# Performance work log

Hardware: AMD Instinct MI355X
Metric: run time of the kernel (lower is better)

## Reference

```python
import jax, jax.numpy as jnp
import numpy as np

T, B, S, K, C = 2, 64, 30, 12, 20
N_ITEMS, D_ITEM, D_RNN = 20000, 128, 256
D_IN = D_ITEM + D_RNN  # cross_mode concatenates h_meta to basket embedding


def gru_cell(x, h, Wih, Whh, bih, bhh):
    # PyTorch GRUCell gate order: r, z, n
    gi = x @ Wih.T + bih
    gh = h @ Whh.T + bhh
    ir, iz, in_ = jnp.split(gi, 3, -1)
    hr, hz, hn = jnp.split(gh, 3, -1)
    r = jax.nn.sigmoid(ir + hr)
    z = jax.nn.sigmoid(iz + hz)
    n = jnp.tanh(in_ + r * hn)
    return (1.0 - z) * n + z * h


def setup_inputs() -> dict:
    key = jax.random.key(0)
    ks = jax.random.split(key, 16)
    def u(k, sh, fan):
        b = 1.0 / np.sqrt(fan)
        return jax.random.uniform(k, sh, jnp.float32, -b, b)
    return {
        "user_vectors": jax.random.randint(ks[0], (B,), 0, 1000),
        "item_vectors": jax.random.randint(ks[1], (T, B, S, K), 0, N_ITEMS),
        "copy_vectors": jax.random.randint(ks[2], (T, B, S, C), 0, N_ITEMS),
        "emb": jax.random.normal(ks[3], (N_ITEMS, D_ITEM), jnp.float32) * 0.05,
        "Wih": u(ks[4], (T, 3 * D_RNN, D_IN), D_RNN),
        "Whh": u(ks[5], (T, 3 * D_RNN, D_RNN), D_RNN),
        "bih": u(ks[6], (T, 3 * D_RNN), D_RNN),
        "bhh": u(ks[7], (T, 3 * D_RNN), D_RNN),
        "mWih": u(ks[8], (3 * D_RNN, T * D_RNN), D_RNN),
        "mWhh": u(ks[9], (3 * D_RNN, D_RNN), D_RNN),
        "mbih": u(ks[10], (3 * D_RNN,), D_RNN),
        "mbhh": u(ks[11], (3 * D_RNN,), D_RNN),
        "Wnew": u(ks[12], (N_ITEMS, D_RNN), D_RNN),
        "bnew": u(ks[13], (N_ITEMS,), D_RNN),
        "Wcopy": u(ks[14], (T, N_ITEMS, D_RNN), D_RNN),
        "bcopy": u(ks[15], (T, N_ITEMS), D_RNN),
    }


def _forward(item_vectors, copy_vectors, emb, Wih, Whh, bih, bhh,
             mWih, mWhh, mbih, mbhh, Wnew, bnew, Wcopy, bcopy):
    emb = emb.at[0].set(0.0)  # padding_idx=0
    e_items = emb[item_vectors]                               # [T,B,S,K,Di]
    valid = (item_vectors > 0).astype(e_items.dtype)          # [T,B,S,K]
    n_basket = valid.sum(-1)                                  # [T,B,S]
    cell_mask = (n_basket > 0).astype(e_items.dtype)          # [T,B,S]
    den = n_basket + (n_basket == 0).astype(e_items.dtype)
    e_baskets = e_items.sum(-2) / den[..., None]              # ave pool [T,B,S,Di]

    xs = jnp.moveaxis(e_baskets, 2, 0)  # [S,T,B,Di]
    ms = jnp.moveaxis(cell_mask, 2, 0)  # [S,T,B]

    h0 = jnp.zeros((T, B, D_RNN), e_items.dtype)
    hm0 = jnp.zeros((B, D_RNN), e_items.dtype)
    task_gru = jax.vmap(gru_cell)  # vmap over the task axis (distinct weights)

    def step(carry, inp):
        h_tasks, h_meta = carry
        x_t, m_t = inp
        # cross_mode: concat current meta hidden onto each task's input
        cell_in = jnp.concatenate(
            [x_t, jnp.broadcast_to(h_meta, (T, B, D_RNN))], -1)  # [T,B,D_IN]
        nh = task_gru(cell_in, h_tasks, Wih, Whh, bih, bhh)
        m = m_t[..., None]
        h_tasks = nh * m + h_tasks * (1.0 - m)  # freeze hidden on empty baskets
        meta_in = jnp.transpose(h_tasks, (1, 0, 2)).reshape(B, T * D_RNN)
        h_meta = gru_cell(meta_in, h_meta, mWih, mWhh, mbih, mbhh)
        return (h_tasks, h_meta), (h_tasks, h_meta)

    _, (h_seq, hm_seq) = jax.lax.scan(step, (h0, hm0), (xs, ms))
    e_rnn_tasks = jnp.transpose(h_seq, (1, 2, 0, 3))  # [T,B,S,H]
    e_rnn_meta = jnp.transpose(hm_seq, (1, 0, 2))     # [B,S,H]

    score_new = jnp.einsum('bsh,nh->bsn', e_rnn_meta, Wnew) + bnew  # [B,S,N]
    ti = jnp.arange(T)[:, None, None, None]
    bi = jnp.arange(B)[None, :, None, None]
    si = jnp.arange(S)[None, None, :, None]
    copy_mask = jnp.zeros((T, B, S, N_ITEMS), score_new.dtype).at[
        ti, bi, si, copy_vectors].set(1.0)  # scatter_(-1, copy_vectors, 1)
    score_copy = (jnp.einsum('tbsh,tnh->tbsn', e_rnn_tasks, Wcopy)
                  + bcopy[:, None, None, :]) * copy_mask  # [T,B,S,N]
    # stack new-item scores with per-task masked copy scores
    return jnp.concatenate([score_new[None], score_copy], 0)  # [T+1,B,S,N]


def reference(user_vectors, item_vectors, copy_vectors, emb, Wih, Whh, bih, bhh,
              mWih, mWhh, mbih, mbhh, Wnew, bnew, Wcopy, bcopy):
    return _forward(item_vectors, copy_vectors, emb, Wih, Whh, bih, bhh,
                    mWih, mWhh, mbih, mbhh, Wnew, bnew, Wcopy, bcopy)
```

## Files before the change

kernel.cpp:

```cpp
#include <hip/hip_runtime.h>

typedef unsigned short u16;
typedef unsigned int u32;
typedef unsigned long long u64;
typedef __attribute__((ext_vector_type(8))) short short8;
typedef __attribute__((ext_vector_type(4))) float f32x4;

#define NB_ 64
#define HELPERS_ 1152

static __device__ __forceinline__ f32x4 mfma16(short8 a, short8 b, f32x4 c) {
  return __builtin_amdgcn_mfma_f32_16x16x32_bf16(a, b, c, 0, 0, 0);
}

static __device__ __forceinline__ void split_bf16(float x, u16& hi, u16& lo) {
  unsigned u = __float_as_uint(x);
  unsigned r = (u + 0x7fffu + ((u >> 16) & 1u)) >> 16;
  hi = (u16)r;
  float fh = __uint_as_float(r << 16);
  float xl = x - fh;
  unsigned ul = __float_as_uint(xl);
  unsigned rl2 = (ul + 0x7fffu + ((ul >> 16) & 1u)) >> 16;
  lo = (u16)rl2;
}

static __device__ __forceinline__ void astore(u32* p, u32 v) {
  __hip_atomic_store(p, v, __ATOMIC_RELAXED, __HIP_MEMORY_SCOPE_AGENT);
}
static __device__ __forceinline__ void unpack8(const uint4& a, const uint4& b,
                                               short8& h, short8& l) {
  u32 wb[8] = {a.x, a.y, a.z, a.w, b.x, b.y, b.z, b.w};
  #pragma unroll
  for (int j = 0; j < 8; ++j) {
    h[j] = (short)(wb[j] & 0xffffu);
    l[j] = (short)(wb[j] >> 16);
  }
}
static __device__ __forceinline__ float unpack_hl(u32 pk) {
  return __uint_as_float((pk & 0xffffu) << 16) + __uint_as_float(pk & 0xffff0000u);
}
static __device__ __forceinline__ void vload8(const u32* p, short8& h, short8& l) {
  uint4 a = *(const uint4*)p;
  uint4 b = *(const uint4*)(p + 4);
  unpack8(a, b, h, l);
}

__global__ __launch_bounds__(128) void k_pool(const int* __restrict__ iv,
                                              const float* __restrict__ emb,
                                              u16* __restrict__ ebh, u16* __restrict__ ebl,
                                              float* __restrict__ cm) {
  int u = blockIdx.x;
  int s = u >> 7;
  int t = (u >> 6) & 1;
  int b = u & 63;
  int d = threadIdx.x;
  const int ibase = ((t * 64 + b) * 30 + s) * 12;
  float sum = 0.f;
  int cnt = 0;
  for (int k = 0; k < 12; ++k) {
    int idx = iv[ibase + k];
    if (idx > 0) { cnt++; sum += emb[(size_t)idx * 128 + d]; }
  }
  float den = (cnt > 0) ? (float)cnt : 1.f;
  float v = sum / den;
  u16 hi, lo; split_bf16(v, hi, lo);
  ebh[(size_t)u * 128 + d] = hi;
  ebl[(size_t)u * 128 + d] = lo;
  if (d == 0) cm[u] = (cnt > 0) ? 1.f : 0.f;
}

__global__ __launch_bounds__(256) void k_swz(const float* __restrict__ Wih,
                                             const float* __restrict__ Whh,
                                             const float* __restrict__ mWih,
                                             const float* __restrict__ mWhh,
                                             const float* __restrict__ Wnew,
                                             u16* __restrict__ w1h, u16* __restrict__ w1l,
                                             u16* __restrict__ w2h, u16* __restrict__ w2l,
                                             u16* __restrict__ wnh, u16* __restrict__ wnl) {
  int gu = blockIdx.x * 4 + (threadIdx.x >> 6);
  int lane = threadIdx.x & 63;
  int ko = (lane >> 4) * 8;
  int cl = lane & 15;
  float src[8];
  if (gu < 2560) {
    int blk = gu / 40, r = gu % 40, ksIdx = r >> 1, nt = r & 1;
    int t = blk >> 5, hd0 = (blk & 31) * 8;
    int c = nt * 16 + cl;
    if (c < 24) {
      int gc = (c < 8) ? (hd0 + c) : (c < 16) ? (256 + hd0 + (c - 8)) : (512 + hd0 + (c - 16));
      const float* wrow; int kk;
      if (ksIdx < 8)       { wrow = Wih + (size_t)(t * 768 + gc) * 384 + 128; kk = ksIdx * 32 + ko; }
      else if (ksIdx < 16) { wrow = Whh + (size_t)(t * 768 + gc) * 256;       kk = (ksIdx - 8) * 32 + ko; }
      else                 { wrow = Wih + (size_t)(t * 768 + gc) * 384;       kk = (ksIdx - 16) * 32 + ko; }
      #pragma unroll
      for (int j = 0; j < 8; ++j) src[j] = wrow[kk + j];
    } else {
      #pragma unroll
      for (int j = 0; j < 8; ++j) src[j] = 0.f;
    }
    int off = gu * 512 + lane * 8;
    #pragma unroll
    for (int j = 0; j < 8; ++j) { u16 h, l; split_bf16(src[j], h, l); w1h[off + j] = h; w1l[off + j] = l; }
  } else if (gu < 4096) {
    int g2 = gu - 2560;
    int blk = g2 / 24, ksIdx = g2 % 24;
    int t1 = blk >> 5;
    int hd0 = blk * 4;
    int c = cl;
    if (c < 12) {
      int gc = (c < 4) ? (hd0 + c) : (c < 8) ? (256 + hd0 + (c - 4)) : (512 + hd0 + (c - 8));
      if (ksIdx < 16) {
        int chunk = (ksIdx < 8) ? (t1 * 8 + ksIdx) : ((1 - t1) * 8 + (ksIdx - 8));
        int kk = chunk * 32 + ko;
        #pragma unroll
        for (int j = 0; j < 8; ++j) src[j] = mWih[(size_t)gc * 512 + kk + j];
      } else {
        int kk = (ksIdx - 16) * 32 + ko;
        #pragma unroll
        for (int j = 0; j < 8; ++j) src[j] = mWhh[(size_t)gc * 256 + kk + j];
      }
    } else {
      #pragma unroll
      for (int j = 0; j < 8; ++j) src[j] = 0.f;
    }
    int off = g2 * 512 + lane * 8;
    #pragma unroll
    for (int j = 0; j < 8; ++j) { u16 h, l; split_bf16(src[j], h, l); w2h[off + j] = h; w2l[off + j] = l; }
  } else if (gu < 14144) {
    int g3 = gu - 4096;
    int gnt = g3 >> 3, ks = g3 & 7;
    int col = gnt * 16 + cl;
    if (col < 20000) {
      int kk = ks * 32 + ko;
      #pragma unroll
      for (int j = 0; j < 8; ++j) src[j] = Wnew[(size_t)col * 256 + kk + j];
    } else {
      #pragma unroll
      for (int j = 0; j < 8; ++j) src[j] = 0.f;
    }
    int off = g3 * 512 + lane * 8;
    #pragma unroll
    for (int j = 0; j < 8; ++j) { u16 h, l; split_bf16(src[j], h, l); wnh[off + j] = h; wnl[off + j] = l; }
  }
}

__global__ __launch_bounds__(256) void k_gix(const u16* __restrict__ ebh, const u16* __restrict__ ebl,
                                             const u16* __restrict__ w1h, const u16* __restrict__ w1l,
                                             const float* __restrict__ bih, const float* __restrict__ bhh,
                                             float* __restrict__ gix) {
  int blk = blockIdx.x;
  int t1 = blk >> 5, hd1 = (blk & 31) * 8;
  int tid = threadIdx.x, lane = tid & 63, w = tid >> 6;
  int arow = w * 16 + (lane & 15);
  int ko = (lane >> 4) * 8;
  __shared__ u16 lwh[4096], lwl[4096];
  {
    const uint4* sh = (const uint4*)(w1h + ((size_t)blk * 40 + 32) * 512);
    const uint4* sl = (const uint4*)(w1l + ((size_t)blk * 40 + 32) * 512);
    uint4* dh = (uint4*)lwh; uint4* dl = (uint4*)lwl;
    for (int i = tid; i < 512; i += 256) { dh[i] = sh[i]; dl[i] = sl[i]; }
  }
  int c = lane & 15;
  float brz, bn = 0.f;
  {
    int gc = (c < 8) ? (hd1 + c) : (256 + hd1 + (c - 8));
    brz = bih[t1 * 768 + gc] + bhh[t1 * 768 + gc];
    if (c < 8) bn = bih[t1 * 768 + 512 + hd1 + c];
  }
  __syncthreads();
  for (int s = 0; s < 30; ++s) {
    f32x4 a3[2];
    a3[0] = (f32x4){0.f, 0.f, 0.f, 0.f};
    a3[1] = (f32x4){0.f, 0.f, 0.f, 0.f};
    const u16* Xh = ebh + (size_t)((s * 2 + t1) * 64 + arow) * 128;
    const u16* Xl = ebl + (size_t)((s * 2 + t1) * 64 + arow) * 128;
    #pragma unroll
    for (int k = 0; k < 4; ++k) {
      short8 xh = *(const short8*)(Xh + k * 32 + ko);
      short8 xl = *(const short8*)(Xl + k * 32 + ko);
      #pragma unroll
      for (int nt = 0; nt < 2; ++nt) {
        short8 bh = *(const short8*)(lwh + (k * 2 + nt) * 512 + lane * 8);
        short8 bl = *(const short8*)(lwl + (k * 2 + nt) * 512 + lane * 8);
        a3[nt] = mfma16(xh, bh, a3[nt]);
        a3[nt] = mfma16(xl, bh, a3[nt]);
        a3[nt] = mfma16(xh, bl, a3[nt]);
      }
    }
    float* grow = gix + (size_t)(blk * 30 + s) * 64 * 32;
    #pragma unroll
    for (int i = 0; i < 4; ++i) {
      int r = w * 16 + (lane >> 4) * 4 + i;
      grow[r * 32 + c] = a3[0][i] + brz;
      if (c < 8) grow[r * 32 + 16 + c] = a3[1][i] + bn;
    }
  }
}

static __device__ __forceinline__ void bar_arrive(u32* slots, int blk, int epoch) {
  __syncthreads();
  if (threadIdx.x == 0) astore(slots + blk, (u32)epoch);
}
static __device__ __forceinline__ void bar_wait(u32* slots, int epoch) {
  int lane = threadIdx.x & 63;
  u32 v;
  for (;;) {
    asm volatile("global_load_dword %0, %1, off sc0 sc1\n\ts_waitcnt vmcnt(0)"
                 : "=v"(v) : "v"(slots + lane) : "memory");
    if ((int)v >= epoch) break;
  }
}

#define RNN_LDS 130560

__global__ __launch_bounds__(256, 1) void k_rnn(
    const u16* __restrict__ w1h, const u16* __restrict__ w1l,
    const u16* __restrict__ w2h, const u16* __restrict__ w2l,
    const float* __restrict__ gix,
    const float* __restrict__ bhh,
    const float* __restrict__ mbih, const float* __restrict__ mbhh,
    const float* __restrict__ cm,
    u32* __restrict__ hpk,
    u32* __restrict__ apk,
    u32* slots,
    float* __restrict__ zout) {
  if (blockIdx.x >= NB_) {
    const size_t totalf4 = 19200000;
    size_t idx = (size_t)(blockIdx.x - NB_) * 256 + threadIdx.x;
    size_t stride = (size_t)HELPERS_ * 256;
    f32x4 z4 = {0.f, 0.f, 0.f, 0.f};
    f32x4* zp = (f32x4*)zout;
    for (size_t i = idx; i < totalf4; i += stride)
      __builtin_nontemporal_store(z4, zp + i);
    return;
  }

  extern __shared__ char smem[];
  u16* lw1h = (u16*)smem;
  u16* lw1l = (u16*)(smem + 32768);
  u16* lw2h = (u16*)(smem + 65536);
  u16* lw2l = (u16*)(smem + 90112);
  float* ls_rz = (float*)(smem + 114688);
  float* ls_gi = (float*)(smem + 118784);
  float* ls_gh = (float*)(smem + 120832);
  float* ls_cm = (float*)(smem + 122880);

  const int blk = blockIdx.x;
  const int tid = threadIdx.x;
  const int lane = tid & 63;
  const int w = tid >> 6;
  const int t1 = blk >> 5;
  const int hd1 = (blk & 31) * 8;
  const int hd2 = blk * 4;
  const int arow = w * 16 + (lane & 15);
  const int ko = (lane >> 4) * 8;
  int epoch = 0;

  {
    const uint4* s1h = (const uint4*)(w1h + (size_t)blk * 40 * 512);
    const uint4* s1l = (const uint4*)(w1l + (size_t)blk * 40 * 512);
    uint4* d1h = (uint4*)lw1h; uint4* d1l = (uint4*)lw1l;
    for (int i = tid; i < 2048; i += 256) { d1h[i] = s1h[i]; d1l[i] = s1l[i]; }
    const uint4* s2h = (const uint4*)(w2h + (size_t)blk * 24 * 512);
    const uint4* s2l = (const uint4*)(w2l + (size_t)blk * 24 * 512);
    uint4* d2h = (uint4*)lw2h; uint4* d2l = (uint4*)lw2l;
    for (int i = tid; i < 1536; i += 256) { d2h[i] = s2h[i]; d2l[i] = s2l[i]; }
    for (int i = tid; i < 1920; i += 256) ls_cm[i] = cm[((i >> 6) * 2 + t1) * 64 + (i & 63)];
  }
  const int cc = lane & 15;
  float bhhn = (cc < 8) ? bhh[t1 * 768 + 512 + hd1 + cc] : 0.f;
  float mrz_b = 0.f, mgi_b = 0.f, mgh_b = 0.f;
  if (cc < 8) {
    int gc = (cc < 4) ? (hd2 + cc) : (256 + hd2 + (cc - 4));
    mrz_b = mbih[gc] + mbhh[gc];
  } else if (cc < 12) {
    int gn = 512 + hd2 + (cc - 8);
    mgi_b = mbih[gn];
    mgh_b = mbhh[gn];
  }

  float gq[8];
  {
    const float* grow = gix + (size_t)(blk * 30 + 0) * 2048;
    #pragma unroll
    for (int i = 0; i < 4; ++i) {
      int r = w * 16 + (lane >> 4) * 4 + i;
      gq[i]     = grow[r * 32 + cc];
      gq[4 + i] = grow[r * 32 + 16 + (cc & 7)];
    }
  }
  __syncthreads();

  short8 ah1[8], al1[8];
  short8 xh2[8], xl2[8];
  f32x4 a2s[2];
  a2s[0] = (f32x4){0.f, 0.f, 0.f, 0.f};
  a2s[1] = (f32x4){0.f, 0.f, 0.f, 0.f};
  float hold0 = 0.f, hold1 = 0.f;
  float hm_reg = 0.f;

  for (int s = 0; s < 30; ++s) {
    f32x4 a1[2];
    a1[0] = (f32x4){0.f, 0.f, 0.f, 0.f};
    a1[1] = (f32x4){0.f, 0.f, 0.f, 0.f};
    if (s > 0) {
      bar_wait(slots, epoch);
      const u32* Ap = apk + (size_t)(arow * 30 + (s - 1)) * 256 + ko;
      uint4 ra[16];
      #pragma unroll
      for (int k = 0; k < 8; ++k) {
        ra[2 * k]     = *(const uint4*)(Ap + k * 32);
        ra[2 * k + 1] = *(const uint4*)(Ap + k * 32 + 4);
      }
      #pragma unroll
      for (int k = 0; k < 8; ++k) {
        unpack8(ra[2 * k], ra[2 * k + 1], ah1[k], al1[k]);
        #pragma unroll
        for (int nt = 0; nt < 2; ++nt) {
          short8 bh = *(const short8*)(lw1h + (k * 2 + nt) * 512 + lane * 8);
          short8 bl = *(const short8*)(lw1l + (k * 2 + nt) * 512 + lane * 8);
          a1[nt] = mfma16(ah1[k], bh, a1[nt]);
          a1[nt] = mfma16(al1[k], bh, a1[nt]);
          a1[nt] = mfma16(ah1[k], bl, a1[nt]);
        }
      }
    }
    #pragma unroll
    for (int i = 0; i < 4; ++i) {
      int rl = (lane >> 4) * 4 + i;
      ls_rz[(w * 16 + rl) * 16 + cc] = a1[0][i] + a2s[0][i] + gq[i];
      if (cc < 8) {
        ls_gi[(w * 16 + rl) * 8 + cc] = a1[1][i] + gq[4 + i];
        ls_gh[(w * 16 + rl) * 8 + cc] = a2s[1][i] + bhhn;
      }
    }
    asm volatile("s_waitcnt lgkmcnt(0)" ::: "memory");
    {
      int item = lane;
      int rl = item >> 3, c = item & 7;
      float rv = ls_rz[(w * 16 + rl) * 16 + c], zv = ls_rz[(w * 16 + rl) * 16 + 8 + c];
      float gi = ls_gi[(w * 16 + rl) * 8 + c], gh = ls_gh[(w * 16 + rl) * 8 + c];
      float r = 1.f / (1.f + expf(-rv));
      float z = 1.f / (1.f + expf(-zv));
      float n = tanhf(gi + r * gh);
      int b = w * 16 + rl;
      float m = ls_cm[s * 64 + b];
      float hnew = (1.f - z) * n + z * hold0;
      float hout = (m > 0.5f) ? hnew : hold0;
      hold0 = hout;
      int oo = (((s + 1) * 2 + t1) * 64 + b) * 256 + hd1 + c;
      u16 xh, xl; split_bf16(hout, xh, xl);
      astore(hpk + oo, (u32)xh | ((u32)xl << 16));
    }
    {
      int item = 64 + lane;
      int rl = item >> 3, c = item & 7;
      float rv = ls_rz[(w * 16 + rl) * 16 + c], zv = ls_rz[(w * 16 + rl) * 16 + 8 + c];
      float gi = ls_gi[(w * 16 + rl) * 8 + c], gh = ls_gh[(w * 16 + rl) * 8 + c];
      float r = 1.f / (1.f + expf(-rv));
      float z = 1.f / (1.f + expf(-zv));
      float n = tanhf(gi + r * gh);
      int b = w * 16 + rl;
      float m = ls_cm[s * 64 + b];
      float hnew = (1.f - z) * n + z * hold1;
      float hout = (m > 0.5f) ? hnew : hold1;
      hold1 = hout;
      int oo = (((s + 1) * 2 + t1) * 64 + b) * 256 + hd1 + c;
      u16 xh, xl; split_bf16(hout, xh, xl);
      astore(hpk + oo, (u32)xh | ((u32)xl << 16));
    }
    ++epoch;
    bar_arrive(slots, blk, epoch);

    f32x4 m1 = (f32x4){0.f, 0.f, 0.f, 0.f};
    f32x4 m2 = (f32x4){0.f, 0.f, 0.f, 0.f};
    if (s > 0) {
      #pragma unroll
      for (int k = 0; k < 8; ++k) {
        short8 bh = *(const short8*)(lw2h + (16 + k) * 512 + lane * 8);
        short8 bl = *(const short8*)(lw2l + (16 + k) * 512 + lane * 8);
        m2 = mfma16(ah1[k], bh, m2);
        m2 = mfma16(al1[k], bh, m2);
        m2 = mfma16(ah1[k], bl, m2);
      }
    }
    if (s < 29) {
      const float* grow = gix + (size_t)(blk * 30 + s + 1) * 2048;
      #pragma unroll
      for (int i = 0; i < 4; ++i) {
        int r = w * 16 + (lane >> 4) * 4 + i;
        gq[i]     = grow[r * 32 + cc];
        gq[4 + i] = grow[r * 32 + 16 + (cc & 7)];
      }
    }
    bar_wait(slots, epoch);

    {
      const u32* Hp = hpk + (size_t)(((s + 1) * 2 + t1) * 64 + arow) * 256 + ko;
      const u32* Hq = hpk + (size_t)(((s + 1) * 2 + (1 - t1)) * 64 + arow) * 256 + ko;
      uint4 rx[16], ry[16];
      #pragma unroll
      for (int k = 0; k < 8; ++k) {
        rx[2 * k]     = *(const uint4*)(Hp + k * 32);
        rx[2 * k + 1] = *(const uint4*)(Hp + k * 32 + 4);
        ry[2 * k]     = *(const uint4*)(Hq + k * 32);
        ry[2 * k + 1] = *(const uint4*)(Hq + k * 32 + 4);
      }
      #pragma unroll
      for (int k = 0; k < 8; ++k) {
        unpack8(rx[2 * k], rx[2 * k + 1], xh2[k], xl2[k]);
        short8 bh = *(const short8*)(lw2h + k * 512 + lane * 8);
        short8 bl = *(const short8*)(lw2l + k * 512 + lane * 8);
        m1 = mfma16(xh2[k], bh, m1);
        m1 = mfma16(xl2[k], bh, m1);
        m1 = mfma16(xh2[k], bl, m1);
      }
      #pragma unroll
      for (int k = 0; k < 8; ++k) {
        short8 yh, yl;
        unpack8(ry[2 * k], ry[2 * k + 1], yh, yl);
        short8 bh = *(const short8*)(lw2h + (8 + k) * 512 + lane * 8);
        short8 bl = *(const short8*)(lw2l + (8 + k) * 512 + lane * 8);
        m1 = mfma16(yh, bh, m1);
        m1 = mfma16(yl, bh, m1);
        m1 = mfma16(yh, bl, m1);
      }
    }
    #pragma unroll
    for (int i = 0; i < 4; ++i) {
      int rl = (lane >> 4) * 4 + i;
      if (cc < 8) {
        ls_rz[(w * 16 + rl) * 16 + cc] = m1[i] + m2[i] + mrz_b;
      } else if (cc < 12) {
        ls_gi[(w * 16 + rl) * 8 + (cc - 8)] = m1[i] + mgi_b;
        ls_gh[(w * 16 + rl) * 8 + (cc - 8)] = m2[i] + mgh_b;
      }
    }
    asm volatile("s_waitcnt lgkmcnt(0)" ::: "memory");
    {
      int rl = lane >> 2, c = lane & 3;
      float rv = ls_rz[(w * 16 + rl) * 16 + c], zv = ls_rz[(w * 16 + rl) * 16 + 4 + c];
      float gi = ls_gi[(w * 16 + rl) * 8 + c], gh = ls_gh[(w * 16 + rl) * 8 + c];
      float r = 1.f / (1.f + expf(-rv));
      float z = 1.f / (1.f + expf(-zv));
      float n = tanhf(gi + r * gh);
      int b = w * 16 + rl;
      int g2 = hd2 + c;
      float hmnew = (1.f - z) * n + z * hm_reg;
      hm_reg = hmnew;
      int ar = b * 30 + s;
      u16 xh, xl; split_bf16(hmnew, xh, xl);
      astore(apk + ar * 256 + g2, (u32)xh | ((u32)xl << 16));
    }
    ++epoch;
    bar_arrive(slots, blk, epoch);

    a2s[0] = (f32x4){0.f, 0.f, 0.f, 0.f};
    a2s[1] = (f32x4){0.f, 0.f, 0.f, 0.f};
    if (s < 29) {
      #pragma unroll
      for (int k = 0; k < 8; ++k) {
        #pragma unroll
        for (int nt = 0; nt < 2; ++nt) {
          short8 bh = *(const short8*)(lw1h + ((8 + k) * 2 + nt) * 512 + lane * 8);
          short8 bl = *(const short8*)(lw1l + ((8 + k) * 2 + nt) * 512 + lane * 8);
          a2s[nt] = mfma16(xh2[k], bh, a2s[nt]);
          a2s[nt] = mfma16(xl2[k], bh, a2s[nt]);
          a2s[nt] = mfma16(xh2[k], bl, a2s[nt]);
        }
      }
    }
  }
}

__global__ __launch_bounds__(256) void k_gnew(const u32* __restrict__ apk,
                                              const u16* __restrict__ wnh, const u16* __restrict__ wnl,
                                              const float* __restrict__ bnew,
                                              float* __restrict__ out) {
  int bid = blockIdx.x;
  int mb = bid / 157, nb = bid % 157;
  int tid = threadIdx.x, lane = tid & 63, w = tid >> 6;
  int ko = (lane >> 4) * 8;
  f32x4 acc[2][8];
  #pragma unroll
  for (int mi = 0; mi < 2; ++mi)
    #pragma unroll
    for (int nt = 0; nt < 8; ++nt) acc[mi][nt] = (f32x4){0.f, 0.f, 0.f, 0.f};
  #pragma unroll
  for (int ks = 0; ks < 8; ++ks) {
    short8 ah[2], al[2];
    #pragma unroll
    for (int mi = 0; mi < 2; ++mi) {
      int r = mb * 128 + (w * 2 + mi) * 16 + (lane & 15);
      vload8(apk + (size_t)r * 256 + ks * 32 + ko, ah[mi], al[mi]);
    }
    #pragma unroll
    for (int nt = 0; nt < 8; ++nt) {
      int un = (nb * 8 + nt) * 8 + ks;
      short8 bh = *(const short8*)(wnh + (size_t)un * 512 + lane * 8);
      short8 bl = *(const short8*)(wnl + (size_t)un * 512 + lane * 8);
      #pragma unroll
      for (int mi = 0; mi < 2; ++mi) {
        acc[mi][nt] = mfma16(ah[mi], bh, acc[mi][nt]);
        acc[mi][nt] = mfma16(al[mi], bh, acc[mi][nt]);
        acc[mi][nt] = mfma16(ah[mi], bl, acc[mi][nt]);
      }
    }
  }
  #pragma unroll
  for (int mi = 0; mi < 2; ++mi)
    #pragma unroll
    for (int nt = 0; nt < 8; ++nt) {
      int col = nb * 128 + nt * 16 + (lane & 15);
      if (col < 20000) {
        float bn = bnew[col];
        #pragma unroll
        for (int i = 0; i < 4; ++i) {
          int r = mb * 128 + (w * 2 + mi) * 16 + (lane >> 4) * 4 + i;
          out[(size_t)r * 20000 + col] = acc[mi][nt][i] + bn;
        }
      }
    }
}

__global__ __launch_bounds__(256) void k_copy(const u32* __restrict__ hpk,
                                              const int* __restrict__ cv,
                                              const float* __restrict__ wc,
                                              const float* __restrict__ bc,
                                              float* __restrict__ out) {
  int u = blockIdx.x;
  int t = u / 1920;
  int rem = u % 1920;
  int b = rem / 30, s = rem % 30;
  int tid = threadIdx.x, lane = tid & 63, w = tid >> 6;
  float* orow = out + (size_t)(1 + t) * 38400000 + (size_t)(b * 30 + s) * 20000;
  const u32* hp = hpk + (size_t)(((s + 1) * 2 + t) * 64 + b) * 256;
  uint4 hq = *(const uint4*)(hp + lane * 4);
  float4 h4;
  h4.x = unpack_hl(hq.x); h4.y = unpack_hl(hq.y);
  h4.z = unpack_hl(hq.z); h4.w = unpack_hl(hq.w);
  int base = u * 20;
  for (int c = w; c < 20; c += 4) {
    int idx = cv[base + c];
    const float* wr = wc + ((size_t)t * 20000 + idx) * 256;
    float4 w4 = *(const float4*)(wr + lane * 4);
    float d = h4.x * w4.x + h4.y * w4.y + h4.z * w4.z + h4.w * w4.w;
    #pragma unroll
    for (int m = 32; m >= 1; m >>= 1) d += __shfl_xor(d, m, 64);
    if (lane == 0) orow[idx] = d + bc[t * 20000 + idx];
  }
}

extern "C" void kernel_launch(void* const* d_in, const int* in_sizes, int n_in,
                              void* d_out, int out_size, void* d_ws, size_t ws_size,
                              hipStream_t stream) {
  const int* iv = (const int*)d_in[1];
  const int* cv = (const int*)d_in[2];
  const float* emb = (const float*)d_in[3];
  const float* Wih = (const float*)d_in[4];
  const float* Whh = (const float*)d_in[5];
  const float* bih = (const float*)d_in[6];
  const float* bhh = (const float*)d_in[7];
  const float* mWih = (const float*)d_in[8];
  const float* mWhh = (const float*)d_in[9];
  const float* mbih = (const float*)d_in[10];
  const float* mbhh = (const float*)d_in[11];
  const float* Wnew = (const float*)d_in[12];
  const float* bnew = (const float*)d_in[13];
  const float* Wcopy = (const float*)d_in[14];
  const float* bcopy = (const float*)d_in[15];
  float* out = (float*)d_out;
  char* ws = (char*)d_ws;

  size_t o = 0;
  auto take = [&](size_t sz) { size_t r = o; o += sz; return r; };
  size_t BAR = take(256);
  size_t CM  = take(15360);
  size_t EBH = take(983040);
  size_t EBL = take(983040);
  size_t HPK = take(4063232);
  size_t APK = take(1966080);
  size_t GIX = take(15728640);
  size_t W1H = take(2621440);
  size_t W1L = take(2621440);
  size_t W2H = take(1572864);
  size_t W2L = take(1572864);
  size_t WNH = take(10289152);
  size_t WNL = take(10289152);
  if (ws_size < o) return;

  hipFuncSetAttribute(reinterpret_cast<const void*>(k_rnn),
                      hipFuncAttributeMaxDynamicSharedMemorySize, RNN_LDS);

  hipMemsetAsync(ws + BAR, 0, 256, stream);

  k_pool<<<3840, 128, 0, stream>>>(iv, emb, (u16*)(ws + EBH), (u16*)(ws + EBL), (float*)(ws + CM));
  k_swz<<<3536, 256, 0, stream>>>(Wih, Whh, mWih, mWhh, Wnew,
                                  (u16*)(ws + W1H), (u16*)(ws + W1L),
                                  (u16*)(ws + W2H), (u16*)(ws + W2L),
                                  (u16*)(ws + WNH), (u16*)(ws + WNL));
  k_gix<<<64, 256, 0, stream>>>((const u16*)(ws + EBH), (const u16*)(ws + EBL),
                                (const u16*)(ws + W1H), (const u16*)(ws + W1L),
                                bih, bhh, (float*)(ws + GIX));
  k_rnn<<<NB_ + HELPERS_, 256, RNN_LDS, stream>>>(
      (const u16*)(ws + W1H), (const u16*)(ws + W1L),
      (const u16*)(ws + W2H), (const u16*)(ws + W2L),
      (const float*)(ws + GIX), bhh, mbih, mbhh,
      (const float*)(ws + CM),
      (u32*)(ws + HPK), (u32*)(ws + APK),
      (u32*)(ws + BAR),
      out + 38400000);
  k_gnew<<<2355, 256, 0, stream>>>((const u32*)(ws + APK),
                                   (const u16*)(ws + WNH), (const u16*)(ws + WNL),
                                   bnew, out);
  k_copy<<<3840, 256, 0, stream>>>((const u32*)(ws + HPK), cv, Wcopy, bcopy, out);
}
```

Before: 574.1 us.

## Fuse output GEMM and copy scoring into RNN kernel as epoch-gated helper blocks

The separate new-item GEMM and copy-score kernels are folded into the persistent RNN launch as helper blocks. Each helper zeroes its output rows, then spin-waits (with sleeps) on the RNN barrier epoch for the timestep it needs, so output work overlaps the sequential recurrence instead of running after it. The meta hidden-state buffer is changed to timestep-major so each 128-row GEMM tile depends only on two timesteps. The risk is that waiting helpers each hold a CU (the kernel requests about 130 KB of LDS, so one block per CU) and rely on in-order dispatch to avoid starving the RNN blocks.

Result: faster. 488.9 us (-14.8%).

```diff
diff --git a/kernel.cpp b/kernel.cpp
--- a/kernel.cpp
+++ b/kernel.cpp
@@ -7,7 +7,7 @@
 typedef __attribute__((ext_vector_type(4))) float f32x4;
 
 #define NB_ 64
-#define HELPERS_ 1152
+#define NHELP_ 6195
 
 static __device__ __forceinline__ f32x4 mfma16(short8 a, short8 b, f32x4 c) {
   return __builtin_amdgcn_mfma_f32_16x16x32_bf16(a, b, c, 0, 0, 0);
@@ -210,10 +210,23 @@
     if ((int)v >= epoch) break;
   }
 }
+static __device__ __forceinline__ void helper_wait(u32* slots, int target) {
+  if (threadIdx.x < 64) {
+    u32 v;
+    for (;;) {
+      asm volatile("global_load_dword %0, %1, off sc0 sc1\n\ts_waitcnt vmcnt(0)"
+                   : "=v"(v) : "v"(slots + threadIdx.x) : "memory");
+      if (__all((int)v >= target)) break;
+      __builtin_amdgcn_s_sleep(15);
+      __builtin_amdgcn_s_sleep(15);
+    }
+  }
+  __syncthreads();
+}
 
 #define RNN_LDS 130560
 
-__global__ __launch_bounds__(256, 1) void k_rnn(
+__global__ __launch_bounds__(256, 1) void k_mega(
     const u16* __restrict__ w1h, const u16* __restrict__ w1l,
     const u16* __restrict__ w2h, const u16* __restrict__ w2l,
     const float* __restrict__ gix,
@@ -223,15 +236,88 @@
     u32* __restrict__ hpk,
     u32* __restrict__ apk,
     u32* slots,
-    float* __restrict__ zout) {
+    const u16* __restrict__ wnh, const u16* __restrict__ wnl,
+    const float* __restrict__ bnew,
+    const int* __restrict__ cv,
+    const float* __restrict__ wc,
+    const float* __restrict__ bc,
+    float* __restrict__ out) {
+
   if (blockIdx.x >= NB_) {
-    const size_t totalf4 = 19200000;
-    size_t idx = (size_t)(blockIdx.x - NB_) * 256 + threadIdx.x;
-    size_t stride = (size_t)HELPERS_ * 256;
-    f32x4 z4 = {0.f, 0.f, 0.f, 0.f};
-    f32x4* zp = (f32x4*)zout;
-    for (size_t i = idx; i < totalf4; i += stride)
-      __builtin_nontemporal_store(z4, zp + i);
+    int h = blockIdx.x - NB_;
+    int g = h / 413, r = h % 413;
+    int tid = threadIdx.x, lane = tid & 63, w = tid >> 6;
+    int ko = (lane >> 4) * 8;
+    if (r < 256) {
+      int s = 2 * g + (r >= 128);
+      int rr = r & 127;
+      int t = rr >> 6, b = rr & 63;
+      float* orow = out + (size_t)(1 + t) * 38400000 + (size_t)(b * 30 + s) * 20000;
+      f32x4 z4 = {0.f, 0.f, 0.f, 0.f};
+      f32x4* zp = (f32x4*)orow;
+      for (int i = tid; i < 5000; i += 256)
+        __builtin_nontemporal_store(z4, zp + i);
+      helper_wait(slots, 2 * s + 1);
+      const u32* hp = hpk + (size_t)(((s + 1) * 2 + t) * 64 + b) * 256;
+      uint4 hq = *(const uint4*)(hp + lane * 4);
+      float4 h4;
+      h4.x = unpack_hl(hq.x); h4.y = unpack_hl(hq.y);
+      h4.z = unpack_hl(hq.z); h4.w = unpack_hl(hq.w);
+      int base = ((t * 64 + b) * 30 + s) * 20;
+      for (int c = w; c < 20; c += 4) {
+        int idx = cv[base + c];
+        const float* wr = wc + ((size_t)t * 20000 + idx) * 256;
+        float4 w4 = *(const float4*)(wr + lane * 4);
+        float d = h4.x * w4.x + h4.y * w4.y + h4.z * w4.z + h4.w * w4.w;
+        #pragma unroll
+        for (int m = 32; m >= 1; m >>= 1) d += __shfl_xor(d, m, 64);
+        if (lane == 0) orow[idx] = d + bc[t * 20000 + idx];
+      }
+    } else {
+      int q = g, nb = r - 256;
+      helper_wait(slots, 4 * q + 4);
+      f32x4 acc[2][8];
+      #pragma unroll
+      for (int mi = 0; mi < 2; ++mi)
+        #pragma unroll
+        for (int nt = 0; nt < 8; ++nt) acc[mi][nt] = (f32x4){0.f, 0.f, 0.f, 0.f};
+      #pragma unroll
+      for (int ks = 0; ks < 8; ++ks) {
+        short8 ah[2], al[2];
+        #pragma unroll
+        for (int mi = 0; mi < 2; ++mi) {
+          int rrow = q * 128 + (w * 2 + mi) * 16 + (lane & 15);
+          vload8(apk + (size_t)rrow * 256 + ks * 32 + ko, ah[mi], al[mi]);
+        }
+        #pragma unroll
+        for (int nt = 0; nt < 8; ++nt) {
+          int un = (nb * 8 + nt) * 8 + ks;
+          short8 bh = *(const short8*)(wnh + (size_t)un * 512 + lane * 8);
+          short8 bl = *(const short8*)(wnl + (size_t)un * 512 + lane * 8);
+          #pragma unroll
+          for (int mi = 0; mi < 2; ++mi) {
+            acc[mi][nt] = mfma16(ah[mi], bh, acc[mi][nt]);
+            acc[mi][nt] = mfma16(al[mi], bh, acc[mi][nt]);
+            acc[mi][nt] = mfma16(ah[mi], bl, acc[mi][nt]);
+          }
+        }
+      }
+      #pragma unroll
+      for (int mi = 0; mi < 2; ++mi)
+        #pragma unroll
+        for (int nt = 0; nt < 8; ++nt) {
+          int col = nb * 128 + nt * 16 + (lane & 15);
+          if (col < 20000) {
+            float bn = bnew[col];
+            #pragma unroll
+            for (int i = 0; i < 4; ++i) {
+              int rrow = q * 128 + (w * 2 + mi) * 16 + (lane >> 4) * 4 + i;
+              int sA = rrow >> 6, bA = rrow & 63;
+              out[(size_t)(bA * 30 + sA) * 20000 + col] = acc[mi][nt][i] + bn;
+            }
+          }
+        }
+    }
     return;
   }
 
@@ -305,7 +391,7 @@
     a1[1] = (f32x4){0.f, 0.f, 0.f, 0.f};
     if (s > 0) {
       bar_wait(slots, epoch);
-      const u32* Ap = apk + (size_t)(arow * 30 + (s - 1)) * 256 + ko;
+      const u32* Ap = apk + (size_t)((s - 1) * 64 + arow) * 256 + ko;
       uint4 ra[16];
       #pragma unroll
       for (int k = 0; k < 8; ++k) {
@@ -448,7 +534,7 @@
       int g2 = hd2 + c;
       float hmnew = (1.f - z) * n + z * hm_reg;
       hm_reg = hmnew;
-      int ar = b * 30 + s;
+      int ar = s * 64 + b;
       u16 xh, xl; split_bf16(hmnew, xh, xl);
       astore(apk + ar * 256 + g2, (u32)xh | ((u32)xl << 16));
     }
@@ -470,84 +556,6 @@
         }
       }
     }
-  }
-}
-
-__global__ __launch_bounds__(256) void k_gnew(const u32* __restrict__ apk,
-                                              const u16* __restrict__ wnh, const u16* __restrict__ wnl,
-                                              const float* __restrict__ bnew,
-                                              float* __restrict__ out) {
-  int bid = blockIdx.x;
-  int mb = bid / 157, nb = bid % 157;
-  int tid = threadIdx.x, lane = tid & 63, w = tid >> 6;
-  int ko = (lane >> 4) * 8;
-  f32x4 acc[2][8];
-  #pragma unroll
-  for (int mi = 0; mi < 2; ++mi)
-    #pragma unroll
-    for (int nt = 0; nt < 8; ++nt) acc[mi][nt] = (f32x4){0.f, 0.f, 0.f, 0.f};
-  #pragma unroll
-  for (int ks = 0; ks < 8; ++ks) {
-    short8 ah[2], al[2];
-    #pragma unroll
-    for (int mi = 0; mi < 2; ++mi) {
-      int r = mb * 128 + (w * 2 + mi) * 16 + (lane & 15);
-      vload8(apk + (size_t)r * 256 + ks * 32 + ko, ah[mi], al[mi]);
-    }
-    #pragma unroll
-    for (int nt = 0; nt < 8; ++nt) {
-      int un = (nb * 8 + nt) * 8 + ks;
-      short8 bh = *(const short8*)(wnh + (size_t)un * 512 + lane * 8);
-      short8 bl = *(const short8*)(wnl + (size_t)un * 512 + lane * 8);
-      #pragma unroll
-      for (int mi = 0; mi < 2; ++mi) {
-        acc[mi][nt] = mfma16(ah[mi], bh, acc[mi][nt]);
-        acc[mi][nt] = mfma16(al[mi], bh, acc[mi][nt]);
-        acc[mi][nt] = mfma16(ah[mi], bl, acc[mi][nt]);
-      }
-    }
-  }
-  #pragma unroll
-  for (int mi = 0; mi < 2; ++mi)
-    #pragma unroll
-    for (int nt = 0; nt < 8; ++nt) {
-      int col = nb * 128 + nt * 16 + (lane & 15);
-      if (col < 20000) {
-        float bn = bnew[col];
-        #pragma unroll
-        for (int i = 0; i < 4; ++i) {
-          int r = mb * 128 + (w * 2 + mi) * 16 + (lane >> 4) * 4 + i;
-          out[(size_t)r * 20000 + col] = acc[mi][nt][i] + bn;
-        }
-      }
-    }
-}
-
-__global__ __launch_bounds__(256) void k_copy(const u32* __restrict__ hpk,
-                                              const int* __restrict__ cv,
-                                              const float* __restrict__ wc,
-                                              const float* __restrict__ bc,
-                                              float* __restrict__ out) {
-  int u = blockIdx.x;
-  int t = u / 1920;
-  int rem = u % 1920;
-  int b = rem / 30, s = rem % 30;
-  int tid = threadIdx.x, lane = tid & 63, w = tid >> 6;
-  float* orow = out + (size_t)(1 + t) * 38400000 + (size_t)(b * 30 + s) * 20000;
-  const u32* hp = hpk + (size_t)(((s + 1) * 2 + t) * 64 + b) * 256;
-  uint4 hq = *(const uint4*)(hp + lane * 4);
-  float4 h4;
-  h4.x = unpack_hl(hq.x); h4.y = unpack_hl(hq.y);
-  h4.z = unpack_hl(hq.z); h4.w = unpack_hl(hq.w);
-  int base = u * 20;
-  for (int c = w; c < 20; c += 4) {
-    int idx = cv[base + c];
-    const float* wr = wc + ((size_t)t * 20000 + idx) * 256;
-    float4 w4 = *(const float4*)(wr + lane * 4);
-    float d = h4.x * w4.x + h4.y * w4.y + h4.z * w4.z + h4.w * w4.w;
-    #pragma unroll
-    for (int m = 32; m >= 1; m >>= 1) d += __shfl_xor(d, m, 64);
-    if (lane == 0) orow[idx] = d + bc[t * 20000 + idx];
   }
 }
 
@@ -589,7 +597,7 @@
   size_t WNL = take(10289152);
   if (ws_size < o) return;
 
-  hipFuncSetAttribute(reinterpret_cast<const void*>(k_rnn),
+  hipFuncSetAttribute(reinterpret_cast<const void*>(k_mega),
                       hipFuncAttributeMaxDynamicSharedMemorySize, RNN_LDS);
 
   hipMemsetAsync(ws + BAR, 0, 256, stream);
@@ -602,16 +610,13 @@
   k_gix<<<64, 256, 0, stream>>>((const u16*)(ws + EBH), (const u16*)(ws + EBL),
                                 (const u16*)(ws + W1H), (const u16*)(ws + W1L),
                                 bih, bhh, (float*)(ws + GIX));
-  k_rnn<<<NB_ + HELPERS_, 256, RNN_LDS, stream>>>(
+  k_mega<<<NB_ + NHELP_, 256, RNN_LDS, stream>>>(
       (const u16*)(ws + W1H), (const u16*)(ws + W1L),
       (const u16*)(ws + W2H), (const u16*)(ws + W2L),
       (const float*)(ws + GIX), bhh, mbih, mbhh,
       (const float*)(ws + CM),
       (u32*)(ws + HPK), (u32*)(ws + APK),
       (u32*)(ws + BAR),
-      out + 38400000);
-  k_gnew<<<2355, 256, 0, stream>>>((const u32*)(ws + APK),
-                                   (const u16*)(ws + WNH), (const u16*)(ws + WNL),
-                                   bnew, out);
-  k_copy<<<3840, 256, 0, stream>>>((const u32*)(ws + HPK), cv, Wcopy, bcopy, out);
-}
+      (const u16*)(ws + WNH), (const u16*)(ws + WNL),
+      bnew, cv, Wcopy, bcopy, out);
+}
```
